# Optimization experiments

Measured on AMD Instinct MI355X. Metric: run time of the kernel, lower is better.

## Reference

```python
import jax, jax.numpy as jnp
import numpy as np

N_SRC = 50000
N_DST = 50000
E = 800000
IN_DIM = 128
OUT_DIM = 128
H = 8
DK = OUT_DIM // H  # 16
SLOPE = 0.2  # leaky relu negative slope


def setup_inputs() -> dict:
    key = jax.random.key(0)
    ks = jax.random.split(key, 12)
    std_lin = 0.05  # stand-in for xavier_normal scale
    inp = {
        "feat_src": jax.random.normal(ks[0], (N_SRC, IN_DIM), jnp.float32),
        "feat_dst": jax.random.normal(ks[1], (N_DST, IN_DIM), jnp.float32),
        "src_idx": jax.random.randint(ks[2], (E,), 0, N_SRC, jnp.int32),
        "dst_idx": jnp.sort(jax.random.randint(ks[3], (E,), 0, N_DST, jnp.int32)),
        "Wq": jax.random.normal(ks[4], (OUT_DIM, IN_DIM), jnp.float32) * std_lin,
        "bq": jnp.zeros((OUT_DIM,), jnp.float32),
        "Wk": jax.random.normal(ks[5], (OUT_DIM, IN_DIM), jnp.float32) * std_lin,
        "bk": jnp.zeros((OUT_DIM,), jnp.float32),
        "Wv": jax.random.normal(ks[6], (OUT_DIM, IN_DIM), jnp.float32) * std_lin,
        "bv": jnp.zeros((OUT_DIM,), jnp.float32),
        "relation_att": jax.random.normal(ks[7], (H, DK, DK), jnp.float32) * 0.2,
        "Wo": jax.random.normal(ks[8], (OUT_DIM, OUT_DIM), jnp.float32) * std_lin,
        "bo": jnp.zeros((OUT_DIM,), jnp.float32),
    }
    return inp


def reference(feat_src, feat_dst, src_idx, dst_idx,
              Wq, bq, Wk, bk, Wv, bv, relation_att, Wo, bo):
    n_dst = feat_dst.shape[0]
    # node-level projections, split into heads
    q = (feat_dst @ Wq.T + bq).reshape(-1, H, DK)   # (N_dst, H, DK)
    k = (feat_src @ Wk.T + bk).reshape(-1, H, DK)   # (N_src, H, DK)
    v = (feat_src @ Wv.T + bv).reshape(-1, H, DK)   # (N_src, H, DK)
    # relation-aware transform of keys (per head)
    k = jnp.einsum('nhd,hde->nhe', k, relation_att)  # (N_src, H, DK)
    scale = jnp.sqrt(jnp.asarray(DK, feat_src.dtype))
    # per-edge, per-head attention logits
    logits = jnp.einsum('ehd,ehd->eh', q[dst_idx], k[src_idx]) / scale  # (E, H)
    logits = jnp.where(logits >= 0, logits, SLOPE * logits)             # leaky relu
    # numerically stable edge softmax over incoming edges of each dst
    seg_max = jax.ops.segment_max(logits, dst_idx, num_segments=n_dst)
    seg_max = jnp.where(jnp.isfinite(seg_max), seg_max, 0.0)
    ex = jnp.exp(logits - seg_max[dst_idx])
    denom = jax.ops.segment_sum(ex, dst_idx, num_segments=n_dst)
    a = ex / denom[dst_idx]                                             # (E, H)
    # weighted message aggregation: sum_e v[src_e] * a_e
    msg = v[src_idx] * a[:, :, None]                                    # (E, H, DK)
    h = jax.ops.segment_sum(msg, dst_idx, num_segments=n_dst)           # (N_dst, H, DK)
    out = h.reshape(n_dst, OUT_DIM) @ Wo.T + bo
    return out
```

## Files before the change

### kernel.cpp

```cpp
#include <hip/hip_runtime.h>
#include <math.h>

#define DIM 128
#define H 8
#define DK 16
#define BM 64
#define LDB 136

typedef __attribute__((ext_vector_type(8))) short short8;
typedef __attribute__((ext_vector_type(4))) float f32x4;
typedef unsigned short u16;
typedef unsigned int u32;

__device__ inline u16 f2bf(float f) {
    union { float f; u32 u; } v; v.f = f;
    u32 r = v.u + 0x7fffu + ((v.u >> 16) & 1u);
    return (u16)(r >> 16);
}
__device__ inline float bfl(u32 u) { union { u32 u; float f; } v; v.u = u << 16; return v.f; }
__device__ inline float bfh(u32 u) { union { u32 u; float f; } v; v.u = u & 0xffff0000u; return v.f; }

__global__ __launch_bounds__(256, 4)
void proj_qkv(const float* __restrict__ fsrc, const float* __restrict__ fdst,
              const float* __restrict__ Wq, const float* __restrict__ bq,
              const float* __restrict__ Wk2, const float* __restrict__ bk2,
              const float* __restrict__ Wv, const float* __restrict__ bv,
              u16* __restrict__ qo, u16* __restrict__ kvo,
              int n_dst, int n_src, int gq, int gs) {
    __shared__ __align__(16) u16 wl[DIM * LDB];
    const int bid = blockIdx.x;
    const float *X, *W, *B; u16* Y; int n, tile, ldy, coff;
    if (bid < gq)           { X = fdst; W = Wq;  B = bq;  Y = qo;  n = n_dst; tile = bid;           ldy = 128; coff = 0; }
    else if (bid < gq + gs) { X = fsrc; W = Wk2; B = bk2; Y = kvo; n = n_src; tile = bid - gq;      ldy = 256; coff = 0; }
    else                    { X = fsrc; W = Wv;  B = bv;  Y = kvo; n = n_src; tile = bid - gq - gs; ldy = 256; coff = 128; }

    const int tid = threadIdx.x;
#pragma unroll
    for (int it = 0; it < 8; ++it) {
        int c8 = it * 256 + tid;
        int row = c8 >> 4, ck = c8 & 15;
        const float4* s = (const float4*)&W[(size_t)row * DIM + ck * 8];
        float4 f0 = s[0], f1 = s[1];
        short8 u;
        u[0] = (short)f2bf(f0.x); u[1] = (short)f2bf(f0.y);
        u[2] = (short)f2bf(f0.z); u[3] = (short)f2bf(f0.w);
        u[4] = (short)f2bf(f1.x); u[5] = (short)f2bf(f1.y);
        u[6] = (short)f2bf(f1.z); u[7] = (short)f2bf(f1.w);
        *(short8*)&wl[row * LDB + ck * 8] = u;
    }
    __syncthreads();
    const int lane = tid & 63, wave = tid >> 6;
    const int lrow = lane & 15, kg = lane >> 4;
    const int rbase = tile * BM + wave * 16;
    int xr = rbase + lrow; if (xr > n - 1) xr = n - 1;
    const float* xp = X + (size_t)xr * DIM + kg * 8;

    f32x4 acc[8];
#pragma unroll
    for (int j = 0; j < 8; ++j) acc[j] = (f32x4){0.f, 0.f, 0.f, 0.f};

#pragma unroll
    for (int kc = 0; kc < 4; ++kc) {
        float4 a0 = *(const float4*)(xp + kc * 32);
        float4 a1 = *(const float4*)(xp + kc * 32 + 4);
        short8 af;
        af[0] = (short)f2bf(a0.x); af[1] = (short)f2bf(a0.y);
        af[2] = (short)f2bf(a0.z); af[3] = (short)f2bf(a0.w);
        af[4] = (short)f2bf(a1.x); af[5] = (short)f2bf(a1.y);
        af[6] = (short)f2bf(a1.z); af[7] = (short)f2bf(a1.w);
#pragma unroll
        for (int j = 0; j < 8; ++j) {
            short8 bf = *(const short8*)&wl[(j * 16 + lrow) * LDB + kc * 32 + kg * 8];
            acc[j] = __builtin_amdgcn_mfma_f32_16x16x32_bf16(af, bf, acc[j], 0, 0, 0);
        }
    }
#pragma unroll
    for (int r = 0; r < 4; ++r) {
        int gr = rbase + kg * 4 + r;
        if (gr < n) {
#pragma unroll
            for (int j = 0; j < 8; ++j) {
                int c = j * 16 + lrow;
                Y[(size_t)gr * ldy + coff + c] = f2bf(acc[j][r] + B[c]);
            }
        }
    }
}

__global__ __launch_bounds__(256, 4)
void gemm_mfma_b(const u16* __restrict__ X, const float* __restrict__ W,
                 const float* __restrict__ b, float* __restrict__ Y, int n) {
    __shared__ __align__(16) u16 wl[DIM * LDB];
    const int tid = threadIdx.x;
#pragma unroll
    for (int it = 0; it < 8; ++it) {
        int c8 = it * 256 + tid;
        int row = c8 >> 4, ck = c8 & 15;
        const float4* s = (const float4*)&W[(size_t)row * DIM + ck * 8];
        float4 f0 = s[0], f1 = s[1];
        short8 u;
        u[0] = (short)f2bf(f0.x); u[1] = (short)f2bf(f0.y);
        u[2] = (short)f2bf(f0.z); u[3] = (short)f2bf(f0.w);
        u[4] = (short)f2bf(f1.x); u[5] = (short)f2bf(f1.y);
        u[6] = (short)f2bf(f1.z); u[7] = (short)f2bf(f1.w);
        *(short8*)&wl[row * LDB + ck * 8] = u;
    }
    __syncthreads();
    const int lane = tid & 63, wave = tid >> 6;
    const int lrow = lane & 15, kg = lane >> 4;
    const int rbase = blockIdx.x * BM + wave * 16;
    int xr = rbase + lrow; if (xr > n - 1) xr = n - 1;
    const u16* xp = X + (size_t)xr * DIM + kg * 8;

    f32x4 acc[8];
#pragma unroll
    for (int j = 0; j < 8; ++j) acc[j] = (f32x4){0.f, 0.f, 0.f, 0.f};

#pragma unroll
    for (int kc = 0; kc < 4; ++kc) {
        short8 af = *(const short8*)(xp + kc * 32);
#pragma unroll
        for (int j = 0; j < 8; ++j) {
            short8 bf = *(const short8*)&wl[(j * 16 + lrow) * LDB + kc * 32 + kg * 8];
            acc[j] = __builtin_amdgcn_mfma_f32_16x16x32_bf16(af, bf, acc[j], 0, 0, 0);
        }
    }
#pragma unroll
    for (int r = 0; r < 4; ++r) {
        int gr = rbase + kg * 4 + r;
        if (gr < n) {
#pragma unroll
            for (int j = 0; j < 8; ++j) {
                int c = j * 16 + lrow;
                Y[(size_t)gr * DIM + c] = acc[j][r] + b[c];
            }
        }
    }
}

__global__ void fold_relation(const float* __restrict__ Wk, const float* __restrict__ bk,
                              const float* __restrict__ R, float* __restrict__ Wk2,
                              float* __restrict__ bk2) {
    const int o = blockIdx.x;
    const int t = threadIdx.x;
    const int h = o >> 4, e = o & 15;
    float acc = 0.f;
#pragma unroll
    for (int d = 0; d < DK; ++d)
        acc = fmaf(R[h * 256 + d * 16 + e], Wk[(size_t)(h * 16 + d) * DIM + t], acc);
    Wk2[(size_t)o * DIM + t] = acc;
    if (t == 0) {
        float bb = 0.f;
#pragma unroll
        for (int d = 0; d < DK; ++d) bb = fmaf(R[h * 256 + d * 16 + e], bk[h * 16 + d], bb);
        bk2[o] = bb;
    }
}

__global__ void seg_bounds(const int* __restrict__ didx, int* __restrict__ seg,
                           int E, int n_dst) {
    int e = blockIdx.x * blockDim.x + threadIdx.x;
    if (e >= E) return;
    int d = didx[e];
    int dp = (e == 0) ? -1 : didx[e - 1];
    for (int x = dp + 1; x <= d; ++x) seg[x] = e;
    if (e == E - 1)
        for (int x = d + 1; x <= n_dst; ++x) seg[x] = E;
}

__global__ __launch_bounds__(256, 8)
void edge_attn7(const u16* __restrict__ q, const u16* __restrict__ kv,
                const int* __restrict__ sidx, const int* __restrict__ seg,
                u16* __restrict__ hout, int n_dst) {
    const int wave = threadIdx.x >> 6;
    const int lane = threadIdx.x & 63;
    const int dst = blockIdx.x * 4 + wave;
    if (dst >= n_dst) return;
    const int g = lane >> 3, h = lane & 7;

    const int s0 = seg[dst], s1 = seg[dst + 1];

    const uint4* qp = (const uint4*)q;
    uint4 qa = qp[(size_t)dst * 16 + h * 2];
    uint4 qb = qp[(size_t)dst * 16 + h * 2 + 1];
    float qf[16];
    qf[0]  = bfl(qa.x); qf[1]  = bfh(qa.x); qf[2]  = bfl(qa.y); qf[3]  = bfh(qa.y);
    qf[4]  = bfl(qa.z); qf[5]  = bfh(qa.z); qf[6]  = bfl(qa.w); qf[7]  = bfh(qa.w);
    qf[8]  = bfl(qb.x); qf[9]  = bfh(qb.x); qf[10] = bfl(qb.y); qf[11] = bfh(qb.y);
    qf[12] = bfl(qb.z); qf[13] = bfh(qb.z); qf[14] = bfl(qb.w); qf[15] = bfh(qb.w);

    const uint4* kvp = (const uint4*)kv;

    float ssum = 0.f;
    float acc[16];
#pragma unroll
    for (int j = 0; j < 16; ++j) acc[j] = 0.f;

#pragma unroll 2
    for (int e = s0 + g; e < s1; e += 8) {
        const int row = sidx[e];
        const uint4* kb = kvp + (size_t)row * 32 + h * 2;
        uint4 k0 = kb[0], k1 = kb[1];
        uint4 v0 = kb[16], v1 = kb[17];
        float d = 0.f;
        d = fmaf(bfl(k0.x), qf[0], d);  d = fmaf(bfh(k0.x), qf[1], d);
        d = fmaf(bfl(k0.y), qf[2], d);  d = fmaf(bfh(k0.y), qf[3], d);
        d = fmaf(bfl(k0.z), qf[4], d);  d = fmaf(bfh(k0.z), qf[5], d);
        d = fmaf(bfl(k0.w), qf[6], d);  d = fmaf(bfh(k0.w), qf[7], d);
        d = fmaf(bfl(k1.x), qf[8], d);  d = fmaf(bfh(k1.x), qf[9], d);
        d = fmaf(bfl(k1.y), qf[10], d); d = fmaf(bfh(k1.y), qf[11], d);
        d = fmaf(bfl(k1.z), qf[12], d); d = fmaf(bfh(k1.z), qf[13], d);
        d = fmaf(bfl(k1.w), qf[14], d); d = fmaf(bfh(k1.w), qf[15], d);
        float lg = d * 0.25f;
        lg = (lg >= 0.f) ? lg : 0.2f * lg;
        const float p = __expf(lg);
        ssum += p;
        acc[0]  = fmaf(p, bfl(v0.x), acc[0]);  acc[1]  = fmaf(p, bfh(v0.x), acc[1]);
        acc[2]  = fmaf(p, bfl(v0.y), acc[2]);  acc[3]  = fmaf(p, bfh(v0.y), acc[3]);
        acc[4]  = fmaf(p, bfl(v0.z), acc[4]);  acc[5]  = fmaf(p, bfh(v0.z), acc[5]);
        acc[6]  = fmaf(p, bfl(v0.w), acc[6]);  acc[7]  = fmaf(p, bfh(v0.w), acc[7]);
        acc[8]  = fmaf(p, bfl(v1.x), acc[8]);  acc[9]  = fmaf(p, bfh(v1.x), acc[9]);
        acc[10] = fmaf(p, bfl(v1.y), acc[10]); acc[11] = fmaf(p, bfh(v1.y), acc[11]);
        acc[12] = fmaf(p, bfl(v1.z), acc[12]); acc[13] = fmaf(p, bfh(v1.z), acc[13]);
        acc[14] = fmaf(p, bfl(v1.w), acc[14]); acc[15] = fmaf(p, bfh(v1.w), acc[15]);
    }

#pragma unroll
    for (int j = 0; j < 16; ++j) {
        acc[j] += __shfl_xor(acc[j], 8);
        acc[j] += __shfl_xor(acc[j], 16);
        acc[j] += __shfl_xor(acc[j], 32);
    }
    ssum += __shfl_xor(ssum, 8);
    ssum += __shfl_xor(ssum, 16);
    ssum += __shfl_xor(ssum, 32);

    if (g == 0) {
        const float inv = (ssum > 0.f) ? 1.f / ssum : 0.f;
        u16 o[16];
#pragma unroll
        for (int j = 0; j < 16; ++j) o[j] = f2bf(acc[j] * inv);
        uint4 pa, pb;
        pa.x = (u32)o[0]  | ((u32)o[1]  << 16);
        pa.y = (u32)o[2]  | ((u32)o[3]  << 16);
        pa.z = (u32)o[4]  | ((u32)o[5]  << 16);
        pa.w = (u32)o[6]  | ((u32)o[7]  << 16);
        pb.x = (u32)o[8]  | ((u32)o[9]  << 16);
        pb.y = (u32)o[10] | ((u32)o[11] << 16);
        pb.z = (u32)o[12] | ((u32)o[13] << 16);
        pb.w = (u32)o[14] | ((u32)o[15] << 16);
        ((uint4*)hout)[(size_t)dst * 16 + h * 2]     = pa;
        ((uint4*)hout)[(size_t)dst * 16 + h * 2 + 1] = pb;
    }
}

extern "C" void kernel_launch(void* const* d_in, const int* in_sizes, int n_in,
                              void* d_out, int out_size, void* d_ws, size_t ws_size,
                              hipStream_t stream) {
    const float* feat_src = (const float*)d_in[0];
    const float* feat_dst = (const float*)d_in[1];
    const int*   src_idx  = (const int*)d_in[2];
    const int*   dst_idx  = (const int*)d_in[3];
    const float* Wq = (const float*)d_in[4];
    const float* bq = (const float*)d_in[5];
    const float* Wk = (const float*)d_in[6];
    const float* bk = (const float*)d_in[7];
    const float* Wv = (const float*)d_in[8];
    const float* bv = (const float*)d_in[9];
    const float* R  = (const float*)d_in[10];
    const float* Wo = (const float*)d_in[11];
    const float* bo = (const float*)d_in[12];

    const int n_src = in_sizes[0] / DIM;
    const int n_dst = in_sizes[1] / DIM;
    const int E     = in_sizes[2];

    float* out = (float*)d_out;
    u16* q   = (u16*)d_ws;
    u16* kv  = q  + (size_t)n_dst * DIM;
    u16* hag = kv + (size_t)n_src * 2 * DIM;
    int* seg = (int*)(hag + (size_t)n_dst * DIM);
    size_t segEnd = ((size_t)(n_dst + 1) + 3) & ~(size_t)3;
    float* Wk2 = (float*)(seg + segEnd);
    float* bk2 = Wk2 + DIM * DIM;

    const int gq = (n_dst + BM - 1) / BM;
    const int gs = (n_src + BM - 1) / BM;

    seg_bounds<<<(E + 255) / 256, 256, 0, stream>>>(dst_idx, seg, E, n_dst);
    fold_relation<<<DIM, DIM, 0, stream>>>(Wk, bk, R, Wk2, bk2);
    proj_qkv<<<gq + 2 * gs, 256, 0, stream>>>(feat_src, feat_dst, Wq, bq, Wk2, bk2,
                                              Wv, bv, q, kv, n_dst, n_src, gq, gs);
    edge_attn7<<<(n_dst + 3) / 4, 256, 0, stream>>>(q, kv, src_idx, seg, hag, n_dst);
    gemm_mfma_b<<<gq, 256, 0, stream>>>(hag, Wo, bo, out, n_dst);
}
```

Before: 103.7 us.

## Store keys as fp8 in packed KV records and fuse K/V projection

Keys are now stored in fp8 (e4m3 via hardware pack and convert) while values stay bf16, in a 384-byte per-source record holding K then V. This cuts per-edge gather bytes from 64 to 48 per head. The K and V projections are merged into one block that loads the input tile once, and weight rows are permuted so each lane writes contiguous 8-element vectors. The risk is accuracy loss in the attention logits from fp8 keys.

```diff
diff --git a/kernel.cpp b/kernel.cpp
--- a/kernel.cpp
+++ b/kernel.cpp
@@ -2,15 +2,16 @@
 #include <math.h>
 
 #define DIM 128
-#define H 8
-#define DK 16
 #define BM 64
 #define LDB 136
+#define KVREC 384
 
 typedef __attribute__((ext_vector_type(8))) short short8;
 typedef __attribute__((ext_vector_type(4))) float f32x4;
+typedef __attribute__((ext_vector_type(2))) float f32x2;
 typedef unsigned short u16;
 typedef unsigned int u32;
+typedef unsigned char u8;
 
 __device__ inline u16 f2bf(float f) {
     union { float f; u32 u; } v; v.f = f;
@@ -20,20 +21,198 @@
 __device__ inline float bfl(u32 u) { union { u32 u; float f; } v; v.u = u << 16; return v.f; }
 __device__ inline float bfh(u32 u) { union { u32 u; float f; } v; v.u = u & 0xffff0000u; return v.f; }
 
+#define DEC_FMA(w, q0, q1, q2, q3, d) {                          \
+    f32x2 lo_ = __builtin_amdgcn_cvt_pk_f32_fp8((w), false);     \
+    f32x2 hi_ = __builtin_amdgcn_cvt_pk_f32_fp8((w), true);      \
+    d = fmaf(lo_.x, q0, d); d = fmaf(lo_.y, q1, d);              \
+    d = fmaf(hi_.x, q2, d); d = fmaf(hi_.y, q3, d); }
+
+#define PACK8(x0,x1,x2,x3,x4,x5,x6,x7, out) {                    \
+    int d0_ = __builtin_amdgcn_cvt_pk_fp8_f32(x0, x1, 0, false); \
+    d0_ = __builtin_amdgcn_cvt_pk_fp8_f32(x2, x3, d0_, true);    \
+    int d1_ = __builtin_amdgcn_cvt_pk_fp8_f32(x4, x5, 0, false); \
+    d1_ = __builtin_amdgcn_cvt_pk_fp8_f32(x6, x7, d1_, true);    \
+    out.x = (u32)d0_; out.y = (u32)d1_; }
+
+__global__ void fold_relation_kv(const float* __restrict__ Wk, const float* __restrict__ bk,
+                                 const float* __restrict__ Wv, const float* __restrict__ bv,
+                                 const float* __restrict__ R, float* __restrict__ Wkv,
+                                 float* __restrict__ bkv) {
+    const int o = blockIdx.x;
+    const int t = threadIdx.x;
+    if (o < 128) {
+        const int h = o >> 4, e = o & 15;
+        float acc = 0.f;
+#pragma unroll
+        for (int d = 0; d < 16; ++d)
+            acc = fmaf(R[h * 256 + d * 16 + e], Wk[(size_t)(h * 16 + d) * DIM + t], acc);
+        Wkv[(size_t)o * DIM + t] = acc;
+        if (t == 0) {
+            float bb = 0.f;
+#pragma unroll
+            for (int d = 0; d < 16; ++d) bb = fmaf(R[h * 256 + d * 16 + e], bk[h * 16 + d], bb);
+            bkv[o] = bb;
+        }
+    } else {
+        Wkv[(size_t)o * DIM + t] = Wv[(size_t)(o - 128) * DIM + t];
+        if (t == 0) bkv[o] = bv[o - 128];
+    }
+}
+
+__global__ void seg_bounds(const int* __restrict__ didx, int* __restrict__ seg,
+                           int E, int n_dst) {
+    int e = blockIdx.x * blockDim.x + threadIdx.x;
+    if (e >= E) return;
+    int d = didx[e];
+    int dp = (e == 0) ? -1 : didx[e - 1];
+    for (int x = dp + 1; x <= d; ++x) seg[x] = e;
+    if (e == E - 1)
+        for (int x = d + 1; x <= n_dst; ++x) seg[x] = E;
+}
+
 __global__ __launch_bounds__(256, 4)
-void proj_qkv(const float* __restrict__ fsrc, const float* __restrict__ fdst,
+void proj_all(const float* __restrict__ fsrc, const float* __restrict__ fdst,
               const float* __restrict__ Wq, const float* __restrict__ bq,
-              const float* __restrict__ Wk2, const float* __restrict__ bk2,
-              const float* __restrict__ Wv, const float* __restrict__ bv,
-              u16* __restrict__ qo, u16* __restrict__ kvo,
-              int n_dst, int n_src, int gq, int gs) {
+              const float* __restrict__ Wkv, const float* __restrict__ bkv,
+              u16* __restrict__ qo, u8* __restrict__ kvo,
+              int n_dst, int n_src, int gq) {
     __shared__ __align__(16) u16 wl[DIM * LDB];
     const int bid = blockIdx.x;
-    const float *X, *W, *B; u16* Y; int n, tile, ldy, coff;
-    if (bid < gq)           { X = fdst; W = Wq;  B = bq;  Y = qo;  n = n_dst; tile = bid;           ldy = 128; coff = 0; }
-    else if (bid < gq + gs) { X = fsrc; W = Wk2; B = bk2; Y = kvo; n = n_src; tile = bid - gq;      ldy = 256; coff = 0; }
-    else                    { X = fsrc; W = Wv;  B = bv;  Y = kvo; n = n_src; tile = bid - gq - gs; ldy = 256; coff = 128; }
-
+    const bool isQ = bid < gq;
+    const int tile = isQ ? bid : bid - gq;
+    const float* X = isQ ? fdst : fsrc;
+    const int n = isQ ? n_dst : n_src;
+
+    const int tid = threadIdx.x;
+    const int lane = tid & 63, wave = tid >> 6;
+    const int lrow = lane & 15, kg = lane >> 4;
+    const int rbase = tile * BM + wave * 16;
+    int xr = rbase + lrow; if (xr > n - 1) xr = n - 1;
+    const float* xp = X + (size_t)xr * DIM + kg * 8;
+
+    short8 af[4];
+#pragma unroll
+    for (int kc = 0; kc < 4; ++kc) {
+        float4 a0 = *(const float4*)(xp + kc * 32);
+        float4 a1 = *(const float4*)(xp + kc * 32 + 4);
+        short8 u;
+        u[0] = (short)f2bf(a0.x); u[1] = (short)f2bf(a0.y);
+        u[2] = (short)f2bf(a0.z); u[3] = (short)f2bf(a0.w);
+        u[4] = (short)f2bf(a1.x); u[5] = (short)f2bf(a1.y);
+        u[6] = (short)f2bf(a1.z); u[7] = (short)f2bf(a1.w);
+        af[kc] = u;
+    }
+
+    const float* W0 = isQ ? Wq : Wkv;
+#pragma unroll
+    for (int it = 0; it < 8; ++it) {
+        int flat = it * 256 + tid;
+        int c = flat >> 4, ck = flat & 15;
+        int slot = (c & 7) * 16 + (c >> 3);
+        const float4* s = (const float4*)&W0[(size_t)c * DIM + ck * 8];
+        float4 f0 = s[0], f1 = s[1];
+        short8 u;
+        u[0] = (short)f2bf(f0.x); u[1] = (short)f2bf(f0.y);
+        u[2] = (short)f2bf(f0.z); u[3] = (short)f2bf(f0.w);
+        u[4] = (short)f2bf(f1.x); u[5] = (short)f2bf(f1.y);
+        u[6] = (short)f2bf(f1.z); u[7] = (short)f2bf(f1.w);
+        *(short8*)&wl[slot * LDB + ck * 8] = u;
+    }
+    __syncthreads();
+
+    f32x4 acck[8];
+#pragma unroll
+    for (int j = 0; j < 8; ++j) acck[j] = (f32x4){0.f, 0.f, 0.f, 0.f};
+#pragma unroll
+    for (int kc = 0; kc < 4; ++kc)
+#pragma unroll
+        for (int j = 0; j < 8; ++j) {
+            short8 bf = *(const short8*)&wl[(j * 16 + lrow) * LDB + kc * 32 + kg * 8];
+            acck[j] = __builtin_amdgcn_mfma_f32_16x16x32_bf16(af[kc], bf, acck[j], 0, 0, 0);
+        }
+
+    f32x4 accv[8];
+    if (!isQ) {
+        __syncthreads();
+#pragma unroll
+        for (int it = 0; it < 8; ++it) {
+            int flat = it * 256 + tid;
+            int c = flat >> 4, ck = flat & 15;
+            int slot = (c & 7) * 16 + (c >> 3);
+            const float4* s = (const float4*)&Wkv[(size_t)(128 + c) * DIM + ck * 8];
+            float4 f0 = s[0], f1 = s[1];
+            short8 u;
+            u[0] = (short)f2bf(f0.x); u[1] = (short)f2bf(f0.y);
+            u[2] = (short)f2bf(f0.z); u[3] = (short)f2bf(f0.w);
+            u[4] = (short)f2bf(f1.x); u[5] = (short)f2bf(f1.y);
+            u[6] = (short)f2bf(f1.z); u[7] = (short)f2bf(f1.w);
+            *(short8*)&wl[slot * LDB + ck * 8] = u;
+        }
+        __syncthreads();
+#pragma unroll
+        for (int j = 0; j < 8; ++j) accv[j] = (f32x4){0.f, 0.f, 0.f, 0.f};
+#pragma unroll
+        for (int kc = 0; kc < 4; ++kc)
+#pragma unroll
+            for (int j = 0; j < 8; ++j) {
+                short8 bf = *(const short8*)&wl[(j * 16 + lrow) * LDB + kc * 32 + kg * 8];
+                accv[j] = __builtin_amdgcn_mfma_f32_16x16x32_bf16(af[kc], bf, accv[j], 0, 0, 0);
+            }
+    }
+
+    if (isQ) {
+        float bias[8];
+        *(float4*)&bias[0] = *(const float4*)&bq[lrow * 8];
+        *(float4*)&bias[4] = *(const float4*)&bq[lrow * 8 + 4];
+#pragma unroll
+        for (int r = 0; r < 4; ++r) {
+            int gr = rbase + kg * 4 + r;
+            if (gr < n) {
+                u16 o[8];
+#pragma unroll
+                for (int j = 0; j < 8; ++j) o[j] = f2bf(acck[j][r] + bias[j]);
+                uint4 pk;
+                pk.x = (u32)o[0] | ((u32)o[1] << 16);
+                pk.y = (u32)o[2] | ((u32)o[3] << 16);
+                pk.z = (u32)o[4] | ((u32)o[5] << 16);
+                pk.w = (u32)o[6] | ((u32)o[7] << 16);
+                *(uint4*)&qo[(size_t)gr * DIM + lrow * 8] = pk;
+            }
+        }
+    } else {
+        float bk_[8], bv_[8];
+        *(float4*)&bk_[0] = *(const float4*)&bkv[lrow * 8];
+        *(float4*)&bk_[4] = *(const float4*)&bkv[lrow * 8 + 4];
+        *(float4*)&bv_[0] = *(const float4*)&bkv[128 + lrow * 8];
+        *(float4*)&bv_[4] = *(const float4*)&bkv[128 + lrow * 8 + 4];
+#pragma unroll
+        for (int r = 0; r < 4; ++r) {
+            int gr = rbase + kg * 4 + r;
+            if (gr < n) {
+                uint2 kd;
+                PACK8(acck[0][r] + bk_[0], acck[1][r] + bk_[1], acck[2][r] + bk_[2],
+                      acck[3][r] + bk_[3], acck[4][r] + bk_[4], acck[5][r] + bk_[5],
+                      acck[6][r] + bk_[6], acck[7][r] + bk_[7], kd);
+                u16 o[8];
+#pragma unroll
+                for (int j = 0; j < 8; ++j) o[j] = f2bf(accv[j][r] + bv_[j]);
+                uint4 vd;
+                vd.x = (u32)o[0] | ((u32)o[1] << 16);
+                vd.y = (u32)o[2] | ((u32)o[3] << 16);
+                vd.z = (u32)o[4] | ((u32)o[5] << 16);
+                vd.w = (u32)o[6] | ((u32)o[7] << 16);
+                u8* rec = kvo + (size_t)gr * KVREC;
+                *(uint2*)(rec + lrow * 8) = kd;
+                *(uint4*)(rec + 128 + lrow * 16) = vd;
+            }
+        }
+    }
+}
+
+__global__ __launch_bounds__(256, 4)
+void gemm_mfma_b(const u16* __restrict__ X, const float* __restrict__ W,
+                 const float* __restrict__ b, float* __restrict__ Y, int n) {
+    __shared__ __align__(16) u16 wl[DIM * LDB];
     const int tid = threadIdx.x;
 #pragma unroll
     for (int it = 0; it < 8; ++it) {
@@ -51,63 +230,6 @@
     __syncthreads();
     const int lane = tid & 63, wave = tid >> 6;
     const int lrow = lane & 15, kg = lane >> 4;
-    const int rbase = tile * BM + wave * 16;
-    int xr = rbase + lrow; if (xr > n - 1) xr = n - 1;
-    const float* xp = X + (size_t)xr * DIM + kg * 8;
-
-    f32x4 acc[8];
-#pragma unroll
-    for (int j = 0; j < 8; ++j) acc[j] = (f32x4){0.f, 0.f, 0.f, 0.f};
-
-#pragma unroll
-    for (int kc = 0; kc < 4; ++kc) {
-        float4 a0 = *(const float4*)(xp + kc * 32);
-        float4 a1 = *(const float4*)(xp + kc * 32 + 4);
-        short8 af;
-        af[0] = (short)f2bf(a0.x); af[1] = (short)f2bf(a0.y);
-        af[2] = (short)f2bf(a0.z); af[3] = (short)f2bf(a0.w);
-        af[4] = (short)f2bf(a1.x); af[5] = (short)f2bf(a1.y);
-        af[6] = (short)f2bf(a1.z); af[7] = (short)f2bf(a1.w);
-#pragma unroll
-        for (int j = 0; j < 8; ++j) {
-            short8 bf = *(const short8*)&wl[(j * 16 + lrow) * LDB + kc * 32 + kg * 8];
-            acc[j] = __builtin_amdgcn_mfma_f32_16x16x32_bf16(af, bf, acc[j], 0, 0, 0);
-        }
-    }
-#pragma unroll
-    for (int r = 0; r < 4; ++r) {
-        int gr = rbase + kg * 4 + r;
-        if (gr < n) {
-#pragma unroll
-            for (int j = 0; j < 8; ++j) {
-                int c = j * 16 + lrow;
-                Y[(size_t)gr * ldy + coff + c] = f2bf(acc[j][r] + B[c]);
-            }
-        }
-    }
-}
-
-__global__ __launch_bounds__(256, 4)
-void gemm_mfma_b(const u16* __restrict__ X, const float* __restrict__ W,
-                 const float* __restrict__ b, float* __restrict__ Y, int n) {
-    __shared__ __align__(16) u16 wl[DIM * LDB];
-    const int tid = threadIdx.x;
-#pragma unroll
-    for (int it = 0; it < 8; ++it) {
-        int c8 = it * 256 + tid;
-        int row = c8 >> 4, ck = c8 & 15;
-        const float4* s = (const float4*)&W[(size_t)row * DIM + ck * 8];
-        float4 f0 = s[0], f1 = s[1];
-        short8 u;
-        u[0] = (short)f2bf(f0.x); u[1] = (short)f2bf(f0.y);
-        u[2] = (short)f2bf(f0.z); u[3] = (short)f2bf(f0.w);
-        u[4] = (short)f2bf(f1.x); u[5] = (short)f2bf(f1.y);
-        u[6] = (short)f2bf(f1.z); u[7] = (short)f2bf(f1.w);
-        *(short8*)&wl[row * LDB + ck * 8] = u;
-    }
-    __syncthreads();
-    const int lane = tid & 63, wave = tid >> 6;
-    const int lrow = lane & 15, kg = lane >> 4;
     const int rbase = blockIdx.x * BM + wave * 16;
     int xr = rbase + lrow; if (xr > n - 1) xr = n - 1;
     const u16* xp = X + (size_t)xr * DIM + kg * 8;
@@ -138,38 +260,8 @@
     }
 }
 
-__global__ void fold_relation(const float* __restrict__ Wk, const float* __restrict__ bk,
-                              const float* __restrict__ R, float* __restrict__ Wk2,
-                              float* __restrict__ bk2) {
-    const int o = blockIdx.x;
-    const int t = threadIdx.x;
-    const int h = o >> 4, e = o & 15;
-    float acc = 0.f;
-#pragma unroll
-    for (int d = 0; d < DK; ++d)
-        acc = fmaf(R[h * 256 + d * 16 + e], Wk[(size_t)(h * 16 + d) * DIM + t], acc);
-    Wk2[(size_t)o * DIM + t] = acc;
-    if (t == 0) {
-        float bb = 0.f;
-#pragma unroll
-        for (int d = 0; d < DK; ++d) bb = fmaf(R[h * 256 + d * 16 + e], bk[h * 16 + d], bb);
-        bk2[o] = bb;
-    }
-}
-
-__global__ void seg_bounds(const int* __restrict__ didx, int* __restrict__ seg,
-                           int E, int n_dst) {
-    int e = blockIdx.x * blockDim.x + threadIdx.x;
-    if (e >= E) return;
-    int d = didx[e];
-    int dp = (e == 0) ? -1 : didx[e - 1];
-    for (int x = dp + 1; x <= d; ++x) seg[x] = e;
-    if (e == E - 1)
-        for (int x = d + 1; x <= n_dst; ++x) seg[x] = E;
-}
-
 __global__ __launch_bounds__(256, 8)
-void edge_attn7(const u16* __restrict__ q, const u16* __restrict__ kv,
+void edge_attn9(const u16* __restrict__ q, const u8* __restrict__ kv,
                 const int* __restrict__ sidx, const int* __restrict__ seg,
                 u16* __restrict__ hout, int n_dst) {
     const int wave = threadIdx.x >> 6;
@@ -189,8 +281,6 @@
     qf[8]  = bfl(qb.x); qf[9]  = bfh(qb.x); qf[10] = bfl(qb.y); qf[11] = bfh(qb.y);
     qf[12] = bfl(qb.z); qf[13] = bfh(qb.z); qf[14] = bfl(qb.w); qf[15] = bfh(qb.w);
 
-    const uint4* kvp = (const uint4*)kv;
-
     float ssum = 0.f;
     float acc[16];
 #pragma unroll
@@ -199,18 +289,15 @@
 #pragma unroll 2
     for (int e = s0 + g; e < s1; e += 8) {
         const int row = sidx[e];
-        const uint4* kb = kvp + (size_t)row * 32 + h * 2;
-        uint4 k0 = kb[0], k1 = kb[1];
-        uint4 v0 = kb[16], v1 = kb[17];
+        const u8* rec = kv + (size_t)row * KVREC;
+        uint4 k4 = *(const uint4*)(rec + h * 16);
+        uint4 v0 = *(const uint4*)(rec + 128 + h * 32);
+        uint4 v1 = *(const uint4*)(rec + 128 + h * 32 + 16);
         float d = 0.f;
-        d = fmaf(bfl(k0.x), qf[0], d);  d = fmaf(bfh(k0.x), qf[1], d);
-        d = fmaf(bfl(k0.y), qf[2], d);  d = fmaf(bfh(k0.y), qf[3], d);
-        d = fmaf(bfl(k0.z), qf[4], d);  d = fmaf(bfh(k0.z), qf[5], d);
-        d = fmaf(bfl(k0.w), qf[6], d);  d = fmaf(bfh(k0.w), qf[7], d);
-        d = fmaf(bfl(k1.x), qf[8], d);  d = fmaf(bfh(k1.x), qf[9], d);
-        d = fmaf(bfl(k1.y), qf[10], d); d = fmaf(bfh(k1.y), qf[11], d);
-        d = fmaf(bfl(k1.z), qf[12], d); d = fmaf(bfh(k1.z), qf[13], d);
-        d = fmaf(bfl(k1.w), qf[14], d); d = fmaf(bfh(k1.w), qf[15], d);
+        DEC_FMA(k4.x, qf[0],  qf[1],  qf[2],  qf[3],  d);
+        DEC_FMA(k4.y, qf[4],  qf[5],  qf[6],  qf[7],  d);
+        DEC_FMA(k4.z, qf[8],  qf[9],  qf[10], qf[11], d);
+        DEC_FMA(k4.w, qf[12], qf[13], qf[14], qf[15], d);
         float lg = d * 0.25f;
         lg = (lg >= 0.f) ? lg : 0.2f * lg;
         const float p = __expf(lg);
@@ -277,20 +364,20 @@
 
     float* out = (float*)d_out;
     u16* q   = (u16*)d_ws;
-    u16* kv  = q  + (size_t)n_dst * DIM;
-    u16* hag = kv + (size_t)n_src * 2 * DIM;
+    u8*  kv  = (u8*)(q + (size_t)n_dst * DIM);
+    u16* hag = (u16*)(kv + (size_t)n_src * KVREC);
     int* seg = (int*)(hag + (size_t)n_dst * DIM);
     size_t segEnd = ((size_t)(n_dst + 1) + 3) & ~(size_t)3;
-    float* Wk2 = (float*)(seg + segEnd);
-    float* bk2 = Wk2 + DIM * DIM;
+    float* Wkv = (float*)(seg + segEnd);
+    float* bkv = Wkv + 256 * DIM;
 
     const int gq = (n_dst + BM - 1) / BM;
     const int gs = (n_src + BM - 1) / BM;
 
     seg_bounds<<<(E + 255) / 256, 256, 0, stream>>>(dst_idx, seg, E, n_dst);
-    fold_relation<<<DIM, DIM, 0, stream>>>(Wk, bk, R, Wk2, bk2);
-    proj_qkv<<<gq + 2 * gs, 256, 0, stream>>>(feat_src, feat_dst, Wq, bq, Wk2, bk2,
-                                              Wv, bv, q, kv, n_dst, n_src, gq, gs);
-    edge_attn7<<<(n_dst + 3) / 4, 256, 0, stream>>>(q, kv, src_idx, seg, hag, n_dst);
+    fold_relation_kv<<<256, DIM, 0, stream>>>(Wk, bk, Wv, bv, R, Wkv, bkv);
+    proj_all<<<gq + gs, 256, 0, stream>>>(feat_src, feat_dst, Wq, bq, Wkv, bkv,
+                                          q, kv, n_dst, n_src, gq);
+    edge_attn9<<<(n_dst + 3) / 4, 256, 0, stream>>>(q, kv, src_idx, seg, hag, n_dst);
     gemm_mfma_b<<<gq, 256, 0, stream>>>(hag, Wo, bo, out, n_dst);
 }
```

Result: faster. 101.5 us (-2.1%).
